# Kernel tuning notes

Measured on AMD Instinct MI355X. Metric: run time of the kernel, lower is better.

The kernel has to match this reference:

```python
import jax, jax.numpy as jnp
import numpy as np

EDGE = 32          # ImageEdge
KPOOL = 16         # pool_kernel_size = ImageEdge // 2
POOLED = 17        # 1 + ImageEdge - pool_kernel_size
NH = 12            # num_attention_heads
HD = 64            # head_dim
HID = 768          # hidden_size
SR = 2             # ScaleRatio


def setup_inputs() -> dict:
    key = jax.random.key(0)
    k1, k2, k3, k4 = jax.random.split(key, 4)
    B, Q = 8, 2048
    return {
        "image_hidden_states": jax.random.normal(k1, (B, EDGE * EDGE, HID), jnp.float32),
        "text_hidden_states": jax.random.normal(k2, (B, Q, HID), jnp.float32),
        "W_in": jax.random.normal(k3, (HID, HID), jnp.float32) * 0.02,   # input_proj (no bias)
        "W_up": jax.random.normal(k4, (HD, HD * SR * SR), jnp.float32) * 0.02,  # up_proj (no bias)
    }


def reference(image_hidden_states, text_hidden_states, W_in, W_up):
    img, txt = image_hidden_states, text_hidden_states
    B, S, HSZ = img.shape            # S = 1024
    Q = txt.shape[1]
    residual = img

    # cross-attention: text queries attend over image keys
    q = txt.reshape(B, Q, NH, HD).transpose(0, 2, 1, 3)   # [B,H,Q,D]
    k = img.reshape(B, S, NH, HD).transpose(0, 2, 1, 3)   # [B,H,S,D]
    attn = jnp.einsum('bhqd,bhkd->bhqk', q, k) / jnp.sqrt(jnp.float32(HD))
    attn = jax.nn.softmax(attn, axis=-1)                  # [B,H,Q,S]
    # dropout is identity in eval mode

    # pooled attention saliency map
    image_attn = attn.sum(axis=2).reshape(B, NH, EDGE, EDGE)
    pooled = jax.lax.reduce_window(
        image_attn, 0.0, jax.lax.add,
        window_dimensions=(1, 1, KPOOL, KPOOL),
        window_strides=(1, 1, 1, 1), padding='VALID') / (KPOOL * KPOOL)   # [B,H,17,17]
    idx = jnp.argmax(pooled.reshape(B, NH, -1), axis=-1)  # [B,H]
    row = (idx // POOLED).reshape(-1)
    col = (idx % POOLED).reshape(-1)

    # gather the argmax-selected 16x16 region per (batch, head)
    states = img.reshape(B, S, NH, HD).transpose(0, 2, 1, 3)
    states = states.reshape(B * NH, EDGE, EDGE, HD)
    slice_one = lambda s, r, c: jax.lax.dynamic_slice(s, (r, c, 0), (KPOOL, KPOOL, HD))
    region = jax.vmap(slice_one)(states, row, col)        # [B*H,16,16,D]

    # pixel-shuffle upsample back to 32x32
    up = region @ W_up                                    # [B*H,16,16,4*D]
    up = up.reshape(B, NH, KPOOL, KPOOL, SR, SR, HD)
    up = up.transpose(0, 1, 2, 4, 3, 5, 6)                # [B,H,16,2,16,2,D]
    up = up.reshape(B, NH, EDGE * EDGE, HD)
    out = up.transpose(0, 2, 1, 3).reshape(B, EDGE * EDGE, HSZ)

    # dense proj + gelu + residual
    out = jax.nn.gelu(out @ W_in, approximate=False)
    return residual + out
```

## Files before the change

### kernel.cpp

```cpp
#include <hip/hip_runtime.h>
#include <cstdint>
#include <cstddef>

#define BB    8
#define NH    12
#define BH    96
#define SS    1024
#define QQ    2048
#define DD    64
#define HID   768
#define EDGE  32
#define KPOOL 16
#define POOLED 17

typedef short bf16x8 __attribute__((ext_vector_type(8)));
typedef _Float16 f16x8 __attribute__((ext_vector_type(8)));
typedef float f32x4  __attribute__((ext_vector_type(4)));

#define MFMA16B(a, b, c) __builtin_amdgcn_mfma_f32_16x16x32_bf16((a), (b), (c), 0, 0, 0)
#define MFMA16H(a, b, c) __builtin_amdgcn_mfma_f32_16x16x32_f16((a), (b), (c), 0, 0, 0)

#define QSCALE 0.18033688011112042f

#if __has_builtin(__builtin_amdgcn_exp2f)
#define EXP2(x) __builtin_amdgcn_exp2f(x)
#else
#define EXP2(x) exp2f(x)
#endif

__device__ __forceinline__ short f2bf(float x) {
    unsigned u = __builtin_bit_cast(unsigned, x);
    u = u + 0x7fffu + ((u >> 16) & 1u);
    return (short)(u >> 16);
}
__device__ __forceinline__ f16x8 ash(bf16x8 v) {
    return __builtin_bit_cast(f16x8, v);
}

__device__ __forceinline__ size_t fragaddr(int row, int k) {
    return ((size_t)(row >> 4) * 24 + (k >> 5)) * 512 + ((k >> 3) & 3) * 128
         + (row & 15) * 8 + (k & 7);
}


__global__ __launch_bounds__(256) void k_castk(const float* __restrict__ img,
                                               short* __restrict__ Ks) {
    int i = blockIdx.x * 256 + threadIdx.x;
    int quad = i & 3, kh = (i >> 2) & 1;
    int row = i >> 3;
    int c = row & 15, g = row >> 4;
    int s = row & 1023, bh = row >> 10;
    int b = bh / NH, h = bh - b * NH;
    const float* sp = img + ((size_t)b * SS + s) * HID + h * DD + kh * 32 + quad * 8;
    bf16x8 vh;
#pragma unroll
    for (int j = 0; j < 8; j++) {
        _Float16 hi = (_Float16)sp[j];
        vh[j] = __builtin_bit_cast(short, hi);
    }
    *(bf16x8*)(Ks + (size_t)g * 2048 + kh * 512 + quad * 128 + c * 8) = vh;
}

__global__ __launch_bounds__(256) void k_castw(const float* __restrict__ W,
                                               const float* __restrict__ Wup,
                                               short* __restrict__ Wt,
                                               short* __restrict__ Wupb) {
    if (blockIdx.x == 144) {
        for (int i = threadIdx.x; i < 16384; i += 256) {
            int k = i >> 8, n = i & 255;
            int addr = (n >> 4) * 1024 + (k >> 5) * 512 + ((k >> 3) & 3) * 128
                     + (n & 15) * 8 + (k & 7);
            Wupb[addr] = f2bf(Wup[k * 256 + n]);
        }
        return;
    }
    __shared__ float T[64][65];
    int bx = blockIdx.x % 12, by = blockIdx.x / 12;
    for (int i = threadIdx.x; i < 4096; i += 256) {
        int r = i >> 6, cc = i & 63;
        T[r][cc] = W[(size_t)(by * 64 + r) * HID + bx * 64 + cc];
    }
    __syncthreads();
    for (int i = threadIdx.x; i < 4096; i += 256) {
        int r = i >> 6, cc = i & 63;
        int n = bx * 64 + r, k = by * 64 + cc;
        Wt[fragaddr(n, k)] = f2bf(T[cc][r]);
    }
}

__global__ __launch_bounds__(512) void k_fused(const float* __restrict__ txt,
                                               const short* __restrict__ Ks,
                                               float* __restrict__ iattn) {
    __shared__ short Kt[2][8192];
    __shared__ float iacc[2][1024];
    __shared__ float Lred[2][4][16];

    int m = blockIdx.x;
    int bh = ((m >> 9) << 3) | (m & 7);
    int qb = (m >> 3) & 63;
    int tid = threadIdx.x;
    int w = tid >> 6, lane = tid & 63;
    int qi = w >> 2, si = w & 3;
    int quad = lane >> 4, c = lane & 15;
    int b = bh / NH, h = bh - b * NH;

    int q = qb * 32 + qi * 16 + c;
    const float* sp = txt + ((size_t)b * QQ + q) * HID + h * DD + quad * 8;
    f16x8 a0, a1;
#pragma unroll
    for (int j = 0; j < 8; j++) {
        a0[j] = (_Float16)(sp[j] * QSCALE);
        a1[j] = (_Float16)(sp[32 + j] * QSCALE);
    }

    const short* kbase = Ks + (size_t)bh * SS * 128;
    size_t s0 = (size_t)(tid >> 7) * 2048 + (size_t)(tid & 127) * 8;
    int i1 = tid + 512;
    size_t s1 = (size_t)(i1 >> 7) * 2048 + (size_t)(i1 & 127) * 8;

    f32x4 pt[16];
    bf16x8 st0 = *(const bf16x8*)(kbase + s0);
    bf16x8 st1 = *(const bf16x8*)(kbase + s1);

#pragma unroll
    for (int cc = 0; cc < 8; cc++) {
        int buf = cc & 1;
        *(bf16x8*)(&Kt[buf][tid * 8]) = st0;
        *(bf16x8*)(&Kt[buf][(tid + 512) * 8]) = st1;
        if (cc + 1 < 8) {
            st0 = *(const bf16x8*)(kbase + (size_t)(cc + 1) * 16384 + s0);
            st1 = *(const bf16x8*)(kbase + (size_t)(cc + 1) * 16384 + s1);
        }
        __syncthreads();
#pragma unroll
        for (int hh = 0; hh < 2; hh++) {
            const short* kp = &Kt[buf][(si + hh * 4) * 1024 + lane * 8];
            f16x8 kb0 = ash(*(const bf16x8*)(kp));
            f16x8 kb1 = ash(*(const bf16x8*)(kp + 512));
            f32x4 acc = (f32x4){0.f, 0.f, 0.f, 0.f};
            acc = MFMA16H(a0, kb0, acc);
            acc = MFMA16H(a1, kb1, acc);
#pragma unroll
            for (int r = 0; r < 4; r++) pt[cc * 2 + hh][r] = EXP2(acc[r]);
        }
    }

    float rl[4];
#pragma unroll
    for (int r = 0; r < 4; r++) {
        float v = 0.f;
#pragma unroll
        for (int cc = 0; cc < 16; cc++) v += pt[cc][r];
        v += __shfl_xor(v, 1);
        v += __shfl_xor(v, 2);
        v += __shfl_xor(v, 4);
        v += __shfl_xor(v, 8);
        if (c == 0) Lred[qi][si][quad * 4 + r] = v;
    }
    __syncthreads();
#pragma unroll
    for (int r = 0; r < 4; r++)
        rl[r] = __builtin_amdgcn_rcpf(
            Lred[qi][0][quad * 4 + r] + Lred[qi][1][quad * 4 + r] +
            Lred[qi][2][quad * 4 + r] + Lred[qi][3][quad * 4 + r]);

#pragma unroll
    for (int cc = 0; cc < 8; cc++) {
#pragma unroll
        for (int hh = 0; hh < 2; hh++) {
            float v = pt[cc * 2 + hh][0] * rl[0] + pt[cc * 2 + hh][1] * rl[1]
                    + pt[cc * 2 + hh][2] * rl[2] + pt[cc * 2 + hh][3] * rl[3];
            v += __shfl_xor(v, 16);
            v += __shfl_xor(v, 32);
            if (lane < 16) iacc[qi][cc * 128 + (si + hh * 4) * 16 + lane] = v;
        }
    }
    __syncthreads();
    for (int i = tid; i < 1024; i += 512)
        atomicAdd(&iattn[(size_t)bh * SS + i], iacc[0][i] + iacc[1][i]);
}

__global__ __launch_bounds__(256, 2) void k_up(const float* __restrict__ img,
                                               const float* __restrict__ iattn,
                                               const short* __restrict__ Wupb,
                                               short* __restrict__ Xb) {
    __shared__ short Reg[16384];
    float* F = (float*)Reg;
    float* Apool = F;
    float* Vp = F + 1024;
    float* bvp = F + 1568;
    int*   bip = (int*)(F + 1824);

    int bh = blockIdx.x >> 2, nq = blockIdx.x & 3;
    int b = bh / NH, h = bh - b * NH;
    int tid = threadIdx.x;
    int w = tid >> 6, lane = tid & 63;
    int quad = lane >> 4, c = lane & 15;

    for (int i = tid; i < 1024; i += 256) Apool[i] = iattn[(size_t)bh * SS + i];
    __syncthreads();
    for (int i = tid; i < POOLED * EDGE; i += 256) {
        int r = i >> 5, cc = i & 31;
        float s = 0.f;
#pragma unroll
        for (int k = 0; k < KPOOL; k++) s += Apool[(r + k) * EDGE + cc];
        Vp[i] = s;
    }
    __syncthreads();
    float best = -1e30f;
    int bidx = 1 << 30;
    for (int i = tid; i < POOLED * POOLED; i += 256) {
        int r = i / POOLED, cc = i - r * POOLED;
        float s = 0.f;
#pragma unroll
        for (int k = 0; k < KPOOL; k++) s += Vp[r * EDGE + cc + k];
        if (s > best || (s == best && i < bidx)) { best = s; bidx = i; }
    }
    bvp[tid] = best;
    bip[tid] = bidx;
    __syncthreads();
    for (int off = 128; off; off >>= 1) {
        if (tid < off) {
            float ov = bvp[tid + off];
            int oi = bip[tid + off];
            if (ov > bvp[tid] || (ov == bvp[tid] && oi < bip[tid])) {
                bvp[tid] = ov;
                bip[tid] = oi;
            }
        }
        __syncthreads();
    }
    int widx = bip[0];
    __syncthreads();
    int r0 = widx / POOLED, c0 = widx - r0 * POOLED;

    for (int p = tid; p < 2048; p += 256) {
        int pos = p >> 3, sub = p & 7;
        int gi = r0 + (pos >> 4), gj = c0 + (pos & 15);
        const float* sp = img + ((size_t)b * SS + gi * EDGE + gj) * HID + h * DD + sub * 8;
        bf16x8 v;
#pragma unroll
        for (int j = 0; j < 8; j++) v[j] = f2bf(sp[j]);
        *(bf16x8*)(&Reg[(pos >> 4) * 1024 + (sub >> 2) * 512 + (sub & 3) * 128 + (pos & 15) * 8]) = v;
    }
    __syncthreads();

    bf16x8 bu[4][2];
#pragma unroll
    for (int u = 0; u < 4; u++) {
#pragma unroll
        for (int kh = 0; kh < 2; kh++)
            bu[u][kh] = *(const bf16x8*)(Wupb + (nq * 4 + u) * 1024 + kh * 512 + lane * 8);
    }

#pragma unroll
    for (int t = 0; t < 4; t++) {
        int g = w * 4 + t;
        bf16x8 a0 = *(const bf16x8*)(&Reg[g * 1024 + lane * 8]);
        bf16x8 a1 = *(const bf16x8*)(&Reg[g * 1024 + 512 + lane * 8]);
#pragma unroll
        for (int u = 0; u < 4; u++) {
            f32x4 acc = (f32x4){0.f, 0.f, 0.f, 0.f};
            acc = MFMA16B(a0, bu[u][0], acc);
            acc = MFMA16B(a1, bu[u][1], acc);
#pragma unroll
            for (int r = 0; r < 4; r++) {
                int pos = g * 16 + quad * 4 + r;
                int oc = nq * 64 + u * 16 + c;
                int i16 = pos >> 4, j16 = pos & 15;
                int a = oc >> 7, bbit = (oc >> 6) & 1, dp = oc & 63;
                int p2 = (2 * i16 + a) * EDGE + (2 * j16 + bbit);
                int row = b * SS + p2, kdim = h * DD + dp;
                Xb[fragaddr(row, kdim)] = f2bf(acc[r]);
            }
        }
    }
}

__global__ __launch_bounds__(256) void k_out(const short* __restrict__ Xb,
                                             const short* __restrict__ Wt,
                                             const float* __restrict__ img,
                                             float* __restrict__ out) {
    __shared__ short At[2][4096];
    __shared__ short Bt[2][2048];
    int mblk = blockIdx.x & 63, nblk = blockIdx.x >> 6;
    int tid = threadIdx.x;
    int w = tid >> 6, lane = tid & 63;
    int quad = lane >> 4, c = lane & 15;
    int gm0 = mblk * 8, gn0 = nblk * 4;
    int m0 = mblk * 128, n0 = nblk * 64;

    int ua1 = tid + 256;
    const short* srcA0 = Xb + ((size_t)(gm0 + (tid >> 6)) * 24) * 512 + (tid & 63) * 8;
    const short* srcA1 = Xb + ((size_t)(gm0 + (ua1 >> 6)) * 24) * 512 + (ua1 & 63) * 8;
    const short* srcB  = Wt + ((size_t)(gn0 + (tid >> 6)) * 24) * 512 + (tid & 63) * 8;

    f32x4 acc[2][4];
#pragma unroll
    for (int t = 0; t < 2; t++)
#pragma unroll
        for (int u = 0; u < 4; u++) acc[t][u] = (f32x4){0.f, 0.f, 0.f, 0.f};

    bf16x8 sa0 = *(const bf16x8*)(srcA0);
    bf16x8 sa1 = *(const bf16x8*)(srcA1);
    bf16x8 sb  = *(const bf16x8*)(srcB);

    for (int kk = 0; kk < 24; kk++) {
        int buf = kk & 1;
        *(bf16x8*)(&At[buf][tid * 8]) = sa0;
        *(bf16x8*)(&At[buf][ua1 * 8]) = sa1;
        *(bf16x8*)(&Bt[buf][tid * 8]) = sb;
        if (kk + 1 < 24) {
            sa0 = *(const bf16x8*)(srcA0 + (kk + 1) * 512);
            sa1 = *(const bf16x8*)(srcA1 + (kk + 1) * 512);
            sb  = *(const bf16x8*)(srcB  + (kk + 1) * 512);
        }
        __syncthreads();
        bf16x8 a0 = *(const bf16x8*)(&At[buf][(2 * w + 0) * 512 + lane * 8]);
        bf16x8 a1 = *(const bf16x8*)(&At[buf][(2 * w + 1) * 512 + lane * 8]);
        bf16x8 b0 = *(const bf16x8*)(&Bt[buf][0 * 512 + lane * 8]);
        bf16x8 b1 = *(const bf16x8*)(&Bt[buf][1 * 512 + lane * 8]);
        bf16x8 b2 = *(const bf16x8*)(&Bt[buf][2 * 512 + lane * 8]);
        bf16x8 b3 = *(const bf16x8*)(&Bt[buf][3 * 512 + lane * 8]);
        acc[0][0] = MFMA16B(a0, b0, acc[0][0]);
        acc[0][1] = MFMA16B(a0, b1, acc[0][1]);
        acc[0][2] = MFMA16B(a0, b2, acc[0][2]);
        acc[0][3] = MFMA16B(a0, b3, acc[0][3]);
        acc[1][0] = MFMA16B(a1, b0, acc[1][0]);
        acc[1][1] = MFMA16B(a1, b1, acc[1][1]);
        acc[1][2] = MFMA16B(a1, b2, acc[1][2]);
        acc[1][3] = MFMA16B(a1, b3, acc[1][3]);
    }

#pragma unroll
    for (int t = 0; t < 2; t++) {
#pragma unroll
        for (int u = 0; u < 4; u++) {
#pragma unroll
            for (int r = 0; r < 4; r++) {
                int row = m0 + w * 32 + t * 16 + quad * 4 + r;
                int col = n0 + u * 16 + c;
                float x = acc[t][u][r];
                float g = 0.5f * x * (1.f + erff(x * 0.70710678118654752f));
                size_t o = (size_t)row * HID + col;
                out[o] = img[o] + g;
            }
        }
    }
}

extern "C" void kernel_launch(void* const* d_in, const int* in_sizes, int n_in,
                              void* d_out, int out_size, void* d_ws, size_t ws_size,
                              hipStream_t stream) {
    const float* img = (const float*)d_in[0];
    const float* txt = (const float*)d_in[1];
    const float* Win = (const float*)d_in[2];
    const float* Wup = (const float*)d_in[3];
    float* out = (float*)d_out;

    char* w = (char*)d_ws;
    short* Ks    = (short*)(w + 50331648);
    short* Wt    = (short*)(w + 75497472);
    float* iattn = (float*)(w + 77463552);
    short* Wupb  = (short*)(w + 77856768);
    short* Xb    = (short*)(w);

    k_castk<<<dim3(3072), dim3(256), 0, stream>>>(img, Ks);
    k_castw<<<dim3(145), dim3(256), 0, stream>>>(Win, Wup, Wt, Wupb);
    hipMemsetAsync(iattn, 0, (size_t)BH * SS * sizeof(float), stream);
    k_fused<<<dim3(6144), dim3(512), 0, stream>>>(txt, Ks, iattn);
    k_up<<<dim3(384), dim3(256), 0, stream>>>(img, iattn, Wupb, Xb);
    k_out<<<dim3(768), dim3(256), 0, stream>>>(Xb, Wt, img, out);
}
```

Measured before the change: 262.3 us.

## Load K fragments directly from global and replace atomics with partial-sum reduction

```diff
diff --git a/kernel.cpp b/kernel.cpp
--- a/kernel.cpp
+++ b/kernel.cpp
@@ -90,8 +90,7 @@
 
 __global__ __launch_bounds__(512) void k_fused(const float* __restrict__ txt,
                                                const short* __restrict__ Ks,
-                                               float* __restrict__ iattn) {
-    __shared__ short Kt[2][8192];
+                                               float* __restrict__ Part) {
     __shared__ float iacc[2][1024];
     __shared__ float Lred[2][4][16];
 
@@ -113,36 +112,19 @@
         a1[j] = (_Float16)(sp[32 + j] * QSCALE);
     }
 
-    const short* kbase = Ks + (size_t)bh * SS * 128;
-    size_t s0 = (size_t)(tid >> 7) * 2048 + (size_t)(tid & 127) * 8;
-    int i1 = tid + 512;
-    size_t s1 = (size_t)(i1 >> 7) * 2048 + (size_t)(i1 & 127) * 8;
+    const short* kbase = Ks + (size_t)bh * SS * 128 + lane * 8;
 
     f32x4 pt[16];
-    bf16x8 st0 = *(const bf16x8*)(kbase + s0);
-    bf16x8 st1 = *(const bf16x8*)(kbase + s1);
-
-#pragma unroll
-    for (int cc = 0; cc < 8; cc++) {
-        int buf = cc & 1;
-        *(bf16x8*)(&Kt[buf][tid * 8]) = st0;
-        *(bf16x8*)(&Kt[buf][(tid + 512) * 8]) = st1;
-        if (cc + 1 < 8) {
-            st0 = *(const bf16x8*)(kbase + (size_t)(cc + 1) * 16384 + s0);
-            st1 = *(const bf16x8*)(kbase + (size_t)(cc + 1) * 16384 + s1);
-        }
-        __syncthreads();
-#pragma unroll
-        for (int hh = 0; hh < 2; hh++) {
-            const short* kp = &Kt[buf][(si + hh * 4) * 1024 + lane * 8];
-            f16x8 kb0 = ash(*(const bf16x8*)(kp));
-            f16x8 kb1 = ash(*(const bf16x8*)(kp + 512));
-            f32x4 acc = (f32x4){0.f, 0.f, 0.f, 0.f};
-            acc = MFMA16H(a0, kb0, acc);
-            acc = MFMA16H(a1, kb1, acc);
-#pragma unroll
-            for (int r = 0; r < 4; r++) pt[cc * 2 + hh][r] = EXP2(acc[r]);
-        }
+#pragma unroll
+    for (int cc = 0; cc < 16; cc++) {
+        const short* kp = kbase + (size_t)(cc * 4 + si) * 2048;
+        f16x8 kb0 = ash(*(const bf16x8*)(kp));
+        f16x8 kb1 = ash(*(const bf16x8*)(kp + 512));
+        f32x4 acc = (f32x4){0.f, 0.f, 0.f, 0.f};
+        acc = MFMA16H(a0, kb0, acc);
+        acc = MFMA16H(a1, kb1, acc);
+#pragma unroll
+        for (int r = 0; r < 4; r++) pt[cc][r] = EXP2(acc[r]);
     }
 
     float rl[4];
@@ -165,19 +147,31 @@
             Lred[qi][2][quad * 4 + r] + Lred[qi][3][quad * 4 + r]);
 
 #pragma unroll
-    for (int cc = 0; cc < 8; cc++) {
-#pragma unroll
-        for (int hh = 0; hh < 2; hh++) {
-            float v = pt[cc * 2 + hh][0] * rl[0] + pt[cc * 2 + hh][1] * rl[1]
-                    + pt[cc * 2 + hh][2] * rl[2] + pt[cc * 2 + hh][3] * rl[3];
-            v += __shfl_xor(v, 16);
-            v += __shfl_xor(v, 32);
-            if (lane < 16) iacc[qi][cc * 128 + (si + hh * 4) * 16 + lane] = v;
-        }
-    }
-    __syncthreads();
-    for (int i = tid; i < 1024; i += 512)
-        atomicAdd(&iattn[(size_t)bh * SS + i], iacc[0][i] + iacc[1][i]);
+    for (int cc = 0; cc < 16; cc++) {
+        float v = pt[cc][0] * rl[0] + pt[cc][1] * rl[1]
+                + pt[cc][2] * rl[2] + pt[cc][3] * rl[3];
+        v += __shfl_xor(v, 16);
+        v += __shfl_xor(v, 32);
+        if (lane < 16) iacc[qi][cc * 64 + si * 16 + lane] = v;
+    }
+    __syncthreads();
+    for (int i = tid; i < 1024; i += 512) {
+        size_t j = ((size_t)(bh * 64 + qb)) * 1024 + i;
+        Part[j] = iacc[0][i] + iacc[1][i];
+    }
+}
+
+__global__ __launch_bounds__(256) void k_reduce(const float* __restrict__ Part,
+                                                float* __restrict__ iattn) {
+    int bh = blockIdx.x >> 2, quarter = blockIdx.x & 3;
+    int s = quarter * 256 + threadIdx.x;
+    float v = 0.f;
+#pragma unroll 8
+    for (int qb = 0; qb < 64; qb++) {
+        size_t j = ((size_t)(bh * 64 + qb)) * 1024 + s;
+        v += Part[j];
+    }
+    iattn[(size_t)bh * SS + s] = v;
 }
 
 __global__ __launch_bounds__(256, 2) void k_up(const float* __restrict__ img,
@@ -359,6 +353,7 @@
     float* out = (float*)d_out;
 
     char* w = (char*)d_ws;
+    float* Part  = (float*)(w);
     short* Ks    = (short*)(w + 50331648);
     short* Wt    = (short*)(w + 75497472);
     float* iattn = (float*)(w + 77463552);
@@ -367,8 +362,8 @@
 
     k_castk<<<dim3(3072), dim3(256), 0, stream>>>(img, Ks);
     k_castw<<<dim3(145), dim3(256), 0, stream>>>(Win, Wup, Wt, Wupb);
-    hipMemsetAsync(iattn, 0, (size_t)BH * SS * sizeof(float), stream);
-    k_fused<<<dim3(6144), dim3(512), 0, stream>>>(txt, Ks, iattn);
+    k_fused<<<dim3(6144), dim3(512), 0, stream>>>(txt, Ks, Part);
+    k_reduce<<<dim3(384), dim3(256), 0, stream>>>(Part, iattn);
     k_up<<<dim3(384), dim3(256), 0, stream>>>(img, iattn, Wupb, Xb);
     k_out<<<dim3(768), dim3(256), 0, stream>>>(Xb, Wt, img, out);
 }
```

Result: slower. 290.5 us (+10.8%).
